# Performance work log

Hardware: AMD Instinct MI355X
Metric: run time of the kernel (lower is better)

The kernel has to match this reference:

```python
import jax, jax.numpy as jnp
import numpy as np

B, S, D = 8, 8192, 64
N_HASHES = 8
BUCKET_SIZE = 64
N_BUCKETS = S // BUCKET_SIZE  # 128
SELF_ATTN_VALUE = -5e4  # torch reformer TOKEN_SELF_ATTN_VALUE


def setup_inputs() -> dict:
    key = jax.random.key(0)
    k1, k2, k3 = jax.random.split(key, 3)
    qk = jax.random.normal(k1, (B, S, D), dtype=jnp.float32)
    v = jax.random.normal(k2, (B, S, D), dtype=jnp.float32)
    # LSH random rotations: (dim, n_hashes, n_buckets // 2), shared across batch/heads
    rotations = jax.random.normal(k3, (D, N_HASHES, N_BUCKETS // 2), dtype=jnp.float32)
    return {"qk": qk, "v": v, "rotations": rotations, "query_len": S}


def _look_one_back(x):
    # concatenate each chunk with the preceding chunk (wrapping) along the kv axis
    x_extra = jnp.concatenate([x[:, -1:], x[:, :-1]], axis=1)
    return jnp.concatenate([x, x_extra], axis=2)


def _lsh_bucketed_dots(qk, v, rotations):
    batch, seqlen, dim = qk.shape
    n_buckets = seqlen // BUCKET_SIZE
    # --- hash vectors: rotate, concat with negation, argmax -> bucket ids ---
    rotated = jnp.einsum('btf,fhi->bhti', qk, rotations)           # (B, H, S, nb/2)
    rotated = jnp.concatenate([rotated, -rotated], axis=-1)        # (B, H, S, nb)
    buckets = jnp.argmax(rotated, axis=-1)                         # (B, H, S) int
    offsets = (jnp.arange(N_HASHES) * n_buckets)[None, :, None]    # disjoint per round
    buckets = (buckets + offsets).reshape(batch, -1)               # (B, H*S)

    # --- stable bucket sort via composite key (all keys unique) ---
    ticker = jnp.arange(N_HASHES * seqlen)[None, :]                # (1, H*S)
    buckets_and_t = seqlen * buckets + (ticker % seqlen)
    sticker = jnp.argsort(buckets_and_t, axis=-1)                  # sort permutation
    undo_sort = jnp.argsort(sticker, axis=-1)                      # inverse permutation
    st = sticker % seqlen                                          # original token ids

    # --- gather tokens into bucket order ---
    sqk = jnp.take_along_axis(qk, st[..., None], axis=1)           # (B, H*S, D)
    sv = jnp.take_along_axis(v, st[..., None], axis=1)

    n_chunks = N_HASHES * n_buckets
    bq_t = st.reshape(batch, n_chunks, BUCKET_SIZE)                # (B, C, bs)
    bqk = sqk.reshape(batch, n_chunks, BUCKET_SIZE, dim)
    bv = sv.reshape(batch, n_chunks, BUCKET_SIZE, dim)

    bq = bqk
    bk = bqk / (jnp.linalg.norm(bqk, axis=-1, keepdims=True) + 1e-6)  # unit-length keys

    bk = _look_one_back(bk)       # (B, C, 2*bs, D)
    bv = _look_one_back(bv)
    bkv_t = _look_one_back(bq_t)  # (B, C, 2*bs)

    dots = jnp.einsum('buie,buje->buij', bq, bk) * (dim ** -0.5)   # (B, C, bs, 2*bs)
    self_mask = bq_t[:, :, :, None] == bkv_t[:, :, None, :]
    dots = jnp.where(self_mask, SELF_ATTN_VALUE, dots)
    return dots, undo_sort, bv


def reference(qk, v, rotations, query_len):
    batch, seqlen, dim = qk.shape
    dots, undo_sort, bv = _lsh_bucketed_dots(qk, v, rotations)
    dots_logsumexp = jax.nn.logsumexp(dots, axis=-1, keepdims=True)
    p = jnp.exp(dots - dots_logsumexp)                             # per-bucket softmax
    bo = jnp.einsum('buij,buje->buie', p, bv)                      # (B, C, bs, D)
    so = bo.reshape(batch, -1, dim)                                # (B, H*S, D)
    slogits = dots_logsumexp.reshape(batch, -1)                    # (B, H*S)
    # undo the bucket sort
    o = jnp.take_along_axis(so, undo_sort[..., None], axis=1)
    logits = jnp.take_along_axis(slogits, undo_sort, axis=1)
    o = o.reshape(batch, N_HASHES, seqlen, dim)[:, :, :query_len]
    logits = logits.reshape(batch, N_HASHES, seqlen, 1)[:, :, :query_len]
    # combine across hash rounds, weighted by per-round logsumexp
    probs = jnp.exp(logits - jax.nn.logsumexp(logits, axis=1, keepdims=True))
    out = jnp.sum(o * probs, axis=1)                               # (B, query_len, D)
    return out
```

## Files before the change

### kernel.cpp

```cpp
#include <hip/hip_runtime.h>
#include <math.h>

#define B_  8
#define S_  8192
#define D_  64
#define H_  8
#define NB_ 128
#define NC_ 1024
#define REP_CAP 65536
#define T2_ 2e-3f

typedef _Float16 f16x8 __attribute__((ext_vector_type(8)));
typedef _Float16 f16x2 __attribute__((ext_vector_type(2)));
typedef float    f32x4 __attribute__((ext_vector_type(4)));
typedef unsigned int uint_;

#define MFMA16(A, Bv, C) __builtin_amdgcn_mfma_f32_16x16x32_f16(A, Bv, C, 0, 0, 0)

__global__ __launch_bounds__(256) void prep_rot_kernel(
    const float* __restrict__ rot, _Float16* __restrict__ rotHi,
    _Float16* __restrict__ rotLo, int* __restrict__ cnt)
{
  __shared__ float rs[64 * 64];
  const int tid = threadIdx.x, h = blockIdx.x;
  if (h == 0 && tid == 0) *cnt = 0;
#pragma unroll
  for (int it = 0; it < 16; ++it) {
    const int f = it * 4 + (tid >> 6), i = tid & 63;
    rs[f * 64 + i] = rot[f * 512 + h * 64 + i];
  }
  __syncthreads();
  const int i = tid & 63, grp = tid >> 6;
  _Float16 hi[16], lo[16];
#pragma unroll
  for (int ff = 0; ff < 16; ++ff) {
    const float x = rs[(grp * 16 + ff) * 64 + i];
    hi[ff] = (_Float16)x;
    lo[ff] = (_Float16)(x - (float)hi[ff]);
  }
  f16x8* dH = (f16x8*)(rotHi + h * 4096 + i * 64 + grp * 16);
  f16x8* dL = (f16x8*)(rotLo + h * 4096 + i * 64 + grp * 16);
  dH[0] = ((f16x8*)hi)[0]; dH[1] = ((f16x8*)hi)[1];
  dL[0] = ((f16x8*)lo)[0]; dL[1] = ((f16x8*)lo)[1];
}

__global__ __launch_bounds__(256) void prep_tok_kernel(
    const float* __restrict__ qk, const float* __restrict__ v,
    _Float16* __restrict__ q16, _Float16* __restrict__ kn16,
    _Float16* __restrict__ v16)
{
  const int gt = blockIdx.x * 64 + (threadIdx.x >> 2);
  const int qu = threadIdx.x & 3;
  const size_t off = (size_t)gt * 64 + qu * 16;
  float x[16];
#pragma unroll
  for (int k = 0; k < 4; ++k) ((float4*)x)[k] = ((const float4*)(qk + off))[k];
  float ss = 0.f;
#pragma unroll
  for (int k = 0; k < 16; ++k) ss = fmaf(x[k], x[k], ss);
  ss += __shfl_xor(ss, 1); ss += __shfl_xor(ss, 2);
  const float inv = 0.125f / (sqrtf(ss) + 1e-6f);
  f16x8 qh[2], kn[2];
#pragma unroll
  for (int j = 0; j < 16; ++j) {
    qh[j >> 3][j & 7] = (_Float16)x[j];
    kn[j >> 3][j & 7] = (_Float16)(x[j] * inv);
  }
  ((f16x8*)(q16  + off))[0] = qh[0]; ((f16x8*)(q16  + off))[1] = qh[1];
  ((f16x8*)(kn16 + off))[0] = kn[0]; ((f16x8*)(kn16 + off))[1] = kn[1];
  float y[16];
#pragma unroll
  for (int k = 0; k < 4; ++k) ((float4*)y)[k] = ((const float4*)(v + off))[k];
  f16x8 vv[2];
#pragma unroll
  for (int j = 0; j < 16; ++j) vv[j >> 3][j & 7] = (_Float16)y[j];
  ((f16x8*)(v16 + off))[0] = vv[0]; ((f16x8*)(v16 + off))[1] = vv[1];
}

__global__ __launch_bounds__(256) void hash_kernel(
    const float* __restrict__ qk,
    const _Float16* __restrict__ rotHi, const _Float16* __restrict__ rotLo,
    int* __restrict__ bucket, int* __restrict__ cnt, int2* __restrict__ list)
{
  __shared__ _Float16 rH[64 * 72];
  __shared__ _Float16 rL[64 * 72];
  const int tid  = threadIdx.x;
  const int tile = blockIdx.x & 127;
  const int b    = blockIdx.x >> 7;
  const int lane = tid & 63, w = tid >> 6;
  const int m16  = lane & 15, qd = lane >> 4;

  const int t = tile * 64 + w * 16 + m16;
  f16x8 BH0, BH1, BL0, BL1;
  {
    const float* src = qk + ((size_t)b * S_ + t) * 64 + 8 * qd;
    float x[16];
    ((float4*)x)[0] = ((const float4*)src)[0];
    ((float4*)x)[1] = ((const float4*)(src + 4))[0];
    ((float4*)x)[2] = ((const float4*)(src + 32))[0];
    ((float4*)x)[3] = ((const float4*)(src + 36))[0];
#pragma unroll
    for (int j = 0; j < 8; ++j) {
      const _Float16 h0 = (_Float16)x[j];
      BH0[j] = h0; BL0[j] = (_Float16)(x[j] - (float)h0);
      const _Float16 h1 = (_Float16)x[j + 8];
      BH1[j] = h1; BL1[j] = (_Float16)(x[j + 8] - (float)h1);
    }
  }
  const int srow = tid >> 2, scol = (tid & 3) * 16;
  const uint_ qd16 = (uint_)(qd << 4);

#pragma unroll 1
  for (int h = 0; h < 8; ++h) {
    __syncthreads();
    {
      const _Float16* sH = rotHi + h * 4096 + srow * 64 + scol;
      const _Float16* sL = rotLo + h * 4096 + srow * 64 + scol;
      *(f16x8*)(rH + srow * 72 + scol)     = ((const f16x8*)sH)[0];
      *(f16x8*)(rH + srow * 72 + scol + 8) = ((const f16x8*)sH)[1];
      *(f16x8*)(rL + srow * 72 + scol)     = ((const f16x8*)sL)[0];
      *(f16x8*)(rL + srow * 72 + scol + 8) = ((const f16x8*)sL)[1];
    }
    __syncthreads();

    f32x4 acc[4];
#pragma unroll
    for (int mt = 0; mt < 4; ++mt) acc[mt] = (f32x4){0.f, 0.f, 0.f, 0.f};
#pragma unroll
    for (int mt = 0; mt < 4; ++mt) {
      const _Float16* aH = rH + (16 * mt + m16) * 72 + 8 * qd;
      const _Float16* aL = rL + (16 * mt + m16) * 72 + 8 * qd;
      const f16x8 AH0 = *(const f16x8*)aH;
      const f16x8 AH1 = *(const f16x8*)(aH + 32);
      const f16x8 AL0 = *(const f16x8*)aL;
      const f16x8 AL1 = *(const f16x8*)(aL + 32);
      acc[mt] = MFMA16(AH0, BH0, acc[mt]);
      acc[mt] = MFMA16(AH1, BH1, acc[mt]);
      acc[mt] = MFMA16(AH0, BL0, acc[mt]);
      acc[mt] = MFMA16(AH1, BL1, acc[mt]);
      acc[mt] = MFMA16(AL0, BH0, acc[mt]);
      acc[mt] = MFMA16(AL1, BH1, acc[mt]);
    }

    float v1M = -1e30f, v2M = -1e30f, v1m = 1e30f, v2m = 1e30f;
#pragma unroll
    for (int mt = 0; mt < 4; ++mt)
#pragma unroll
      for (int rg = 0; rg < 4; ++rg) {
        uint_ u = __float_as_uint(acc[mt][rg]);
        u = (u & 0xFFFFFFC0u) | qd16 | (uint_)((mt << 2) | rg);
        const float xk = __uint_as_float(u);
        v2M = __builtin_amdgcn_fmed3f(v1M, v2M, xk);
        v1M = fmaxf(v1M, xk);
        v2m = __builtin_amdgcn_fmed3f(v1m, v2m, xk);
        v1m = fminf(v1m, xk);
      }
#pragma unroll
    for (int off = 16; off <= 32; off <<= 1) {
      const float o1M = __shfl_xor(v1M, off), o2M = __shfl_xor(v2M, off);
      v2M = __builtin_amdgcn_fmed3f(v1M, o1M, fmaxf(v2M, o2M));
      v1M = fmaxf(v1M, o1M);
      const float o1m = __shfl_xor(v1m, off), o2m = __shfl_xor(v2m, off);
      v2m = __builtin_amdgcn_fmed3f(v1m, o1m, fminf(v2m, o2m));
      v1m = fminf(v1m, o1m);
    }
    if (qd == 0) {
      const uint_ cM = __float_as_uint(v1M) & 63u;
      const uint_ cm = __float_as_uint(v1m) & 63u;
      const int ixM = 16 * (int)((cM >> 2) & 3u) + 4 * (int)(cM >> 4) + (int)(cM & 3u);
      const int ixm = 16 * (int)((cm >> 2) & 3u) + 4 * (int)(cm >> 4) + (int)(cm & 3u);
      const int bkt = (v1M >= -v1m) ? ixM : 64 + ixm;
      bucket[((size_t)(b * 8 + h)) * S_ + t] = bkt;
      const bool flag = ((v1M - v2M) < T2_) | ((v2m - v1m) < T2_) |
                        (fabsf(v1M + v1m) < T2_);
      if (flag) {
        const int s = atomicAdd(cnt, 1);
        if (s < REP_CAP) list[s] = make_int2(b * 8 + h, t);
      }
    }
  }
}

__global__ __launch_bounds__(256) void repair_kernel(
    const float* __restrict__ qk, const float* __restrict__ rot,
    const int* __restrict__ cnt, const int2* __restrict__ list,
    int* __restrict__ bucket)
{
  const int n = min(*cnt, REP_CAP);
  const int lane = threadIdx.x & 63;
  const int wid  = (blockIdx.x * 256 + threadIdx.x) >> 6;
  const int nw   = gridDim.x * 4;
  for (int idx = wid; idx < n; idx += nw) {
    const int bh = list[idx].x, t = list[idx].y;
    const int b = bh >> 3, hh = bh & 7;
    const float* qrow = qk + ((size_t)b * S_ + t) * D_;
    const float* rcol = rot + hh * 64 + lane;
    double acc = 0.0;
#pragma unroll 8
    for (int f = 0; f < 64; ++f)
      acc = fma((double)qrow[f], (double)rcol[(size_t)f * 512], acc);
    double vM = acc; int iM = lane;
    double vm = acc; int im = lane;
#pragma unroll
    for (int off = 32; off >= 1; off >>= 1) {
      const double voM = __shfl_xor(vM, off); const int ioM = __shfl_xor(iM, off);
      if (voM > vM || (voM == vM && ioM < iM)) { vM = voM; iM = ioM; }
      const double vom = __shfl_xor(vm, off); const int iom = __shfl_xor(im, off);
      if (vom < vm || (vom == vm && iom < im)) { vm = vom; im = iom; }
    }
    if (lane == 0) {
      const int bkt = (vM >= -vm) ? iM : 64 + im;
      bucket[(size_t)bh * S_ + t] = bkt;
    }
  }
}

__global__ __launch_bounds__(1024) void sort_kernel(
    const int* __restrict__ bucket, int* __restrict__ st)
{
  __shared__ uint_ hist[64 * 128];
  __shared__ unsigned short lb[S_];
  __shared__ int off[128];
  const int tid = threadIdx.x;
  const int bh  = blockIdx.x;
  const size_t base = (size_t)bh * S_;

#pragma unroll
  for (int k = 0; k < 8; ++k) hist[tid + k * 1024] = 0;
  __syncthreads();

#pragma unroll
  for (int k = 0; k < 8; ++k) {
    const int t = k * 1024 + tid;
    const int bk = bucket[base + t];
    lb[t] = (unsigned short)bk;
    const int g = t >> 6;
    atomicAdd(&hist[(g & 63) * 128 + bk], 1u << (16 * (g >> 6)));
  }
  __syncthreads();

  if (tid < 128) {
    uint_ s = 0;
#pragma unroll
    for (int g = 0; g < 64; ++g) {
      const uint_ wv = hist[g * 128 + tid];
      s += (wv & 0xFFFFu) + (wv >> 16);
    }
    off[tid] = (int)s;
  }
  __syncthreads();
  if (tid == 0) {
    int run = 0;
    for (int k = 0; k < 128; ++k) { const int c = off[k]; off[k] = run; run += c; }
  }
  __syncthreads();
  if (tid < 128) {
    uint_ run = (uint_)off[tid];
#pragma unroll
    for (int g = 0; g < 64; ++g) {
      const uint_ wv = hist[g * 128 + tid];
      hist[g * 128 + tid] = (wv & 0xFFFF0000u) | run;
      run += (wv & 0xFFFFu);
    }
#pragma unroll
    for (int g = 0; g < 64; ++g) {
      const uint_ wv = hist[g * 128 + tid];
      hist[g * 128 + tid] = (wv & 0xFFFFu) | (run << 16);
      run += (wv >> 16);
    }
  }
  __syncthreads();

  const int lane = tid & 63, wv_ = tid >> 6;
  const int b = bh >> 3, h = bh & 7;
  const size_t stb = (size_t)b * (H_ * S_) + (size_t)h * S_;
  const unsigned long long ltmask = (1ull << lane) - 1ull;
#pragma unroll
  for (int k = 0; k < 8; ++k) {
    const int g = wv_ * 8 + k;
    const int t = g * 64 + lane;
    const int bk = (int)lb[t];
    unsigned long long same = ~0ull;
#pragma unroll
    for (int bit = 0; bit < 7; ++bit) {
      const unsigned long long m = __ballot((bk >> bit) & 1);
      same &= ((bk >> bit) & 1) ? m : ~m;
    }
    const int rloc = __popcll(same & ltmask);
    const uint_ wd = hist[(g & 63) * 128 + bk];
    const int gbase = (int)((wd >> (16 * (g >> 6))) & 0xFFFFu);
    st[stb + gbase + rloc] = t;
  }
}

__global__ __launch_bounds__(256, 4) void attn_kernel(
    const _Float16* __restrict__ q16, const _Float16* __restrict__ kn16,
    const _Float16* __restrict__ v16, const int* __restrict__ st,
    _Float16* __restrict__ so, float* __restrict__ slog)
{
  __shared__ _Float16 sQ[64 * 72];
  __shared__ _Float16 sK[64 * 72];
  __shared__ _Float16 sP[64 * 136];
  __shared__ int sIds[128];

  const int tid = threadIdx.x;
  const int c   = blockIdx.x & (NC_ - 1);
  const int b   = blockIdx.x >> 10;
  const int cm1 = (c + NC_ - 1) & (NC_ - 1);
  const size_t bst = (size_t)b * (H_ * S_);
  const size_t row0 = bst + (size_t)c * 64;
  const size_t row1 = bst + (size_t)cm1 * 64;

  const int lane = tid & 63;
  const int w    = tid >> 6;
  const int m16  = lane & 15;
  const int qd   = lane >> 4;

  if (tid < 128) sIds[tid] = (tid < 64) ? st[row0 + tid] : st[row1 + tid - 64];

  const int r = tid >> 2, qu = tid & 3;
  {
    const int tok = st[row0 + r];
    const size_t go = ((size_t)b * S_ + tok) * 64 + qu * 16;
    const f16x8* sq = (const f16x8*)(q16 + go);
    *(f16x8*)(sQ + r * 72 + qu * 16)     = sq[0];
    *(f16x8*)(sQ + r * 72 + qu * 16 + 8) = sq[1];
    const f16x8* sk = (const f16x8*)(kn16 + go);
    *(f16x8*)(sK + r * 72 + qu * 16)     = sk[0];
    *(f16x8*)(sK + r * 72 + qu * 16 + 8) = sk[1];
  }
  __syncthreads();

  f32x4 acc[8];
#pragma unroll
  for (int jt = 0; jt < 8; ++jt) acc[jt] = (f32x4){0.f, 0.f, 0.f, 0.f};

  const _Float16* qrow = sQ + (16 * w + m16) * 72;
  const f16x8 a0 = *(const f16x8*)(qrow + 8 * qd);
  const f16x8 a1 = *(const f16x8*)(qrow + 32 + 8 * qd);

#pragma unroll
  for (int jt = 0; jt < 4; ++jt) {
    const _Float16* krow = sK + (16 * jt + m16) * 72;
    const f16x8 b0 = *(const f16x8*)(krow + 8 * qd);
    const f16x8 b1 = *(const f16x8*)(krow + 32 + 8 * qd);
    acc[jt] = MFMA16(a0, b0, acc[jt]);
    acc[jt] = MFMA16(a1, b1, acc[jt]);
  }
  __syncthreads();

  {
    const int tok = st[row1 + r];
    const f16x8* sk = (const f16x8*)(kn16 + ((size_t)b * S_ + tok) * 64 + qu * 16);
    *(f16x8*)(sK + r * 72 + qu * 16)     = sk[0];
    *(f16x8*)(sK + r * 72 + qu * 16 + 8) = sk[1];
  }
  __syncthreads();

#pragma unroll
  for (int jt = 4; jt < 8; ++jt) {
    const _Float16* krow = sK + (16 * (jt - 4) + m16) * 72;
    const f16x8 b0 = *(const f16x8*)(krow + 8 * qd);
    const f16x8 b1 = *(const f16x8*)(krow + 32 + 8 * qd);
    acc[jt] = MFMA16(a0, b0, acc[jt]);
    acc[jt] = MFMA16(a1, b1, acc[jt]);
  }

  const int jp = tid >> 2;
  const int tok0 = sIds[2 * jp], tok1 = sIds[2 * jp + 1];
  f16x8 va[2], vb[2];
  {
    const f16x8* s0 = (const f16x8*)(v16 + ((size_t)b * S_ + tok0) * 64 + qu * 16);
    const f16x8* s1 = (const f16x8*)(v16 + ((size_t)b * S_ + tok1) * 64 + qu * 16);
    va[0] = s0[0]; va[1] = s0[1];
    vb[0] = s1[0]; vb[1] = s1[1];
  }

  int rid[4];
#pragma unroll
  for (int rg = 0; rg < 4; ++rg) rid[rg] = sIds[16 * w + 4 * qd + rg];
  float rmax[4] = {-1e30f, -1e30f, -1e30f, -1e30f};
#pragma unroll
  for (int jt = 0; jt < 8; ++jt) {
    const int cid = sIds[16 * jt + m16];
#pragma unroll
    for (int rg = 0; rg < 4; ++rg) {
      float x = acc[jt][rg];
      if (rid[rg] == cid) x = -5e4f;
      acc[jt][rg] = x;
      rmax[rg] = fmaxf(rmax[rg], x);
    }
  }
#pragma unroll
  for (int rg = 0; rg < 4; ++rg) {
    rmax[rg] = fmaxf(rmax[rg], __shfl_xor(rmax[rg], 1));
    rmax[rg] = fmaxf(rmax[rg], __shfl_xor(rmax[rg], 2));
    rmax[rg] = fmaxf(rmax[rg], __shfl_xor(rmax[rg], 4));
    rmax[rg] = fmaxf(rmax[rg], __shfl_xor(rmax[rg], 8));
  }
  float rsum[4] = {0.f, 0.f, 0.f, 0.f};
#pragma unroll
  for (int jt = 0; jt < 8; ++jt)
#pragma unroll
    for (int rg = 0; rg < 4; ++rg) {
      const float e = __expf(acc[jt][rg] - rmax[rg]);
      acc[jt][rg] = e;
      rsum[rg] += e;
    }
#pragma unroll
  for (int rg = 0; rg < 4; ++rg) {
    rsum[rg] += __shfl_xor(rsum[rg], 1);
    rsum[rg] += __shfl_xor(rsum[rg], 2);
    rsum[rg] += __shfl_xor(rsum[rg], 4);
    rsum[rg] += __shfl_xor(rsum[rg], 8);
  }
  float rinv[4];
#pragma unroll
  for (int rg = 0; rg < 4; ++rg) rinv[rg] = 1.f / rsum[rg];

  const int hh = c >> 7;
  const size_t hb = ((size_t)(b * 8 + hh)) * S_;
  if (m16 == 0) {
#pragma unroll
    for (int rg = 0; rg < 4; ++rg)
      slog[hb + rid[rg]] = rmax[rg] + __logf(rsum[rg]);
  }

#pragma unroll
  for (int jt = 0; jt < 8; ++jt)
#pragma unroll
    for (int rg = 0; rg < 4; ++rg)
      sP[(16 * w + 4 * qd + rg) * 136 + 16 * jt + m16] = (_Float16)acc[jt][rg];

  __syncthreads();

  {
    const int j = 2 * jp;
    _Float16* dst = (j < 64) ? (sK + j) : (sQ + (j - 64));
#pragma unroll
    for (int jj = 0; jj < 16; ++jj) {
      const int d = qu * 16 + jj;
      f16x2 pk; pk[0] = va[jj >> 3][jj & 7]; pk[1] = vb[jj >> 3][jj & 7];
      *(f16x2*)(dst + d * 72) = pk;
    }
  }
  __syncthreads();

  f32x4 oacc[4];
#pragma unroll
  for (int dt = 0; dt < 4; ++dt) oacc[dt] = (f32x4){0.f, 0.f, 0.f, 0.f};
  const _Float16* prow = sP + (16 * w + m16) * 136;
#pragma unroll
  for (int s = 0; s < 4; ++s) {
    const f16x8 ap = *(const f16x8*)(prow + 32 * s + 8 * qd);
    const _Float16* vbase = (s < 2) ? sK : sQ;
    const int col0 = 32 * (s & 1) + 8 * qd;
#pragma unroll
    for (int dt = 0; dt < 4; ++dt) {
      const f16x8 bv = *(const f16x8*)(vbase + (16 * dt + m16) * 72 + col0);
      oacc[dt] = MFMA16(ap, bv, oacc[dt]);
    }
  }

#pragma unroll
  for (int dt = 0; dt < 4; ++dt)
#pragma unroll
    for (int rg = 0; rg < 4; ++rg)
      so[(hb + rid[rg]) * 64 + 16 * dt + m16] = (_Float16)(oacc[dt][rg] * rinv[rg]);
}

__global__ __launch_bounds__(256) void combine_kernel(
    const _Float16* __restrict__ so, const float* __restrict__ slog,
    float* __restrict__ out)
{
  const int gt = blockIdx.x * 4 + (threadIdx.x >> 6);
  const int d  = threadIdx.x & 63;
  const int b  = gt >> 13;
  const int t  = gt & (S_ - 1);

  float l[8];
#pragma unroll
  for (int h = 0; h < 8; ++h)
    l[h] = slog[((size_t)(b * 8 + h)) * S_ + t];
  float m = l[0];
#pragma unroll
  for (int h = 1; h < 8; ++h) m = fmaxf(m, l[h]);
  float wv[8], W = 0.f;
#pragma unroll
  for (int h = 0; h < 8; ++h) { wv[h] = expf(l[h] - m); W += wv[h]; }
  const float iW = 1.f / W;
  float acc = 0.f;
#pragma unroll
  for (int h = 0; h < 8; ++h)
    acc = fmaf(wv[h], (float)so[(((size_t)(b * 8 + h)) * S_ + t) * 64 + d], acc);
  out[(size_t)gt * 64 + d] = acc * iW;
}

extern "C" void kernel_launch(void* const* d_in, const int* in_sizes, int n_in,
                              void* d_out, int out_size, void* d_ws, size_t ws_size,
                              hipStream_t stream)
{
  const float* qk  = (const float*)d_in[0];
  const float* v   = (const float*)d_in[1];
  const float* rot = (const float*)d_in[2];
  float* out = (float*)d_out;

  char* ws = (char*)d_ws;
  const size_t MB = 1ull << 20, KB = 1024;
  int*      bucket = (int*)      (ws + 0 * MB);
  int*      st     = (int*)      (ws + 2 * MB);
  float*    slog   = (float*)    (ws + 4 * MB);
  _Float16* q16    = (_Float16*) (ws + 8 * MB);
  _Float16* kn16   = (_Float16*) (ws + 16 * MB);
  _Float16* v16    = (_Float16*) (ws + 24 * MB);
  _Float16* rotHi  = (_Float16*) (ws + 32 * MB);
  _Float16* rotLo  = (_Float16*) (ws + 32 * MB + 64 * KB);
  int*      cnt    = (int*)      (ws + 32 * MB + 128 * KB);
  int2*     list   = (int2*)     (ws + 32 * MB + 192 * KB);
  _Float16* so     = (_Float16*) (ws + 33 * MB);
  if (ws_size < 98 * MB) return;

  hipLaunchKernelGGL(prep_rot_kernel, dim3(8),           dim3(256),  0, stream, rot, rotHi, rotLo, cnt);
  hipLaunchKernelGGL(prep_tok_kernel, dim3(1024),        dim3(256),  0, stream, qk, v, q16, kn16, v16);
  hipLaunchKernelGGL(hash_kernel,     dim3(8 * 128),     dim3(256),  0, stream, qk, rotHi, rotLo, bucket, cnt, list);
  hipLaunchKernelGGL(repair_kernel,   dim3(128),         dim3(256),  0, stream, qk, rot, cnt, list, bucket);
  hipLaunchKernelGGL(sort_kernel,     dim3(64),          dim3(1024), 0, stream, bucket, st);
  hipLaunchKernelGGL(attn_kernel,     dim3(B_ * NC_),    dim3(256),  0, stream, q16, kn16, v16, st, so, slog);
  hipLaunchKernelGGL(combine_kernel,  dim3(B_ * S_ / 4), dim3(256),  0, stream, so, slog, out);
}
```

Baseline: 207.1 us.

## Restructure attention kernel to keep P in registers and shrink shared memory

The attention kernel now computes the transposed score tile (K as the A operand, Q from registers), so each lane holds a full query row's scores. This lets the softmax reduction use two cross-quad shuffles instead of four per row and lets P be fed straight into the PV MFMA from registers, with no sP staging. Shared memory drops to one reused buffer with a swizzled transposed-V layout, and launch bounds rise to 8 blocks per CU for higher occupancy. In exchange the register permutation and swizzle indexing are harder to follow, and register pressure under the tighter bound may cause spills.

```diff
diff --git a/kernel.cpp b/kernel.cpp
--- a/kernel.cpp
+++ b/kernel.cpp
@@ -293,15 +293,13 @@
   }
 }
 
-__global__ __launch_bounds__(256, 4) void attn_kernel(
+__global__ __launch_bounds__(256, 8) void attn_kernel(
     const _Float16* __restrict__ q16, const _Float16* __restrict__ kn16,
     const _Float16* __restrict__ v16, const int* __restrict__ st,
     _Float16* __restrict__ so, float* __restrict__ slog)
 {
-  __shared__ _Float16 sQ[64 * 72];
-  __shared__ _Float16 sK[64 * 72];
-  __shared__ _Float16 sP[64 * 136];
-  __shared__ int sIds[128];
+  __shared__ _Float16 smem[64 * 136];
+  __shared__ __align__(16) int sIds[128];
 
   const int tid = threadIdx.x;
   const int c   = blockIdx.x & (NC_ - 1);
@@ -318,16 +316,20 @@
 
   if (tid < 128) sIds[tid] = (tid < 64) ? st[row0 + tid] : st[row1 + tid - 64];
 
+  const int rid = st[row0 + 16 * w + m16];
+  f16x8 q0, q1;
+  {
+    const _Float16* qp = q16 + ((size_t)b * S_ + rid) * 64 + 8 * qd;
+    q0 = *(const f16x8*)qp;
+    q1 = *(const f16x8*)(qp + 32);
+  }
+
   const int r = tid >> 2, qu = tid & 3;
   {
     const int tok = st[row0 + r];
-    const size_t go = ((size_t)b * S_ + tok) * 64 + qu * 16;
-    const f16x8* sq = (const f16x8*)(q16 + go);
-    *(f16x8*)(sQ + r * 72 + qu * 16)     = sq[0];
-    *(f16x8*)(sQ + r * 72 + qu * 16 + 8) = sq[1];
-    const f16x8* sk = (const f16x8*)(kn16 + go);
-    *(f16x8*)(sK + r * 72 + qu * 16)     = sk[0];
-    *(f16x8*)(sK + r * 72 + qu * 16 + 8) = sk[1];
+    const f16x8* sk = (const f16x8*)(kn16 + ((size_t)b * S_ + tok) * 64 + qu * 16);
+    *(f16x8*)(smem + r * 72 + qu * 16)     = sk[0];
+    *(f16x8*)(smem + r * 72 + qu * 16 + 8) = sk[1];
   }
   __syncthreads();
 
@@ -335,39 +337,73 @@
 #pragma unroll
   for (int jt = 0; jt < 8; ++jt) acc[jt] = (f32x4){0.f, 0.f, 0.f, 0.f};
 
-  const _Float16* qrow = sQ + (16 * w + m16) * 72;
-  const f16x8 a0 = *(const f16x8*)(qrow + 8 * qd);
-  const f16x8 a1 = *(const f16x8*)(qrow + 32 + 8 * qd);
-
 #pragma unroll
   for (int jt = 0; jt < 4; ++jt) {
-    const _Float16* krow = sK + (16 * jt + m16) * 72;
-    const f16x8 b0 = *(const f16x8*)(krow + 8 * qd);
-    const f16x8 b1 = *(const f16x8*)(krow + 32 + 8 * qd);
-    acc[jt] = MFMA16(a0, b0, acc[jt]);
-    acc[jt] = MFMA16(a1, b1, acc[jt]);
+    const _Float16* krow = smem + (16 * jt + m16) * 72;
+    const f16x8 kb0 = *(const f16x8*)(krow + 8 * qd);
+    const f16x8 kb1 = *(const f16x8*)(krow + 32 + 8 * qd);
+    acc[jt] = MFMA16(kb0, q0, acc[jt]);
+    acc[jt] = MFMA16(kb1, q1, acc[jt]);
   }
   __syncthreads();
 
   {
-    const int tok = st[row1 + r];
+    const int tok = sIds[64 + r];
     const f16x8* sk = (const f16x8*)(kn16 + ((size_t)b * S_ + tok) * 64 + qu * 16);
-    *(f16x8*)(sK + r * 72 + qu * 16)     = sk[0];
-    *(f16x8*)(sK + r * 72 + qu * 16 + 8) = sk[1];
+    *(f16x8*)(smem + r * 72 + qu * 16)     = sk[0];
+    *(f16x8*)(smem + r * 72 + qu * 16 + 8) = sk[1];
   }
   __syncthreads();
 
 #pragma unroll
   for (int jt = 4; jt < 8; ++jt) {
-    const _Float16* krow = sK + (16 * (jt - 4) + m16) * 72;
-    const f16x8 b0 = *(const f16x8*)(krow + 8 * qd);
-    const f16x8 b1 = *(const f16x8*)(krow + 32 + 8 * qd);
-    acc[jt] = MFMA16(a0, b0, acc[jt]);
-    acc[jt] = MFMA16(a1, b1, acc[jt]);
-  }
-
-  const int jp = tid >> 2;
-  const int tok0 = sIds[2 * jp], tok1 = sIds[2 * jp + 1];
+    const _Float16* krow = smem + (16 * (jt - 4) + m16) * 72;
+    const f16x8 kb0 = *(const f16x8*)(krow + 8 * qd);
+    const f16x8 kb1 = *(const f16x8*)(krow + 32 + 8 * qd);
+    acc[jt] = MFMA16(kb0, q0, acc[jt]);
+    acc[jt] = MFMA16(kb1, q1, acc[jt]);
+  }
+
+  float m = -1e30f;
+#pragma unroll
+  for (int jt = 0; jt < 8; ++jt) {
+    const int4 cid = *(const int4*)(sIds + 16 * jt + 4 * qd);
+    float x;
+    x = acc[jt][0]; if (cid.x == rid) x = -5e4f; acc[jt][0] = x; m = fmaxf(m, x);
+    x = acc[jt][1]; if (cid.y == rid) x = -5e4f; acc[jt][1] = x; m = fmaxf(m, x);
+    x = acc[jt][2]; if (cid.z == rid) x = -5e4f; acc[jt][2] = x; m = fmaxf(m, x);
+    x = acc[jt][3]; if (cid.w == rid) x = -5e4f; acc[jt][3] = x; m = fmaxf(m, x);
+  }
+  m = fmaxf(m, __shfl_xor(m, 16));
+  m = fmaxf(m, __shfl_xor(m, 32));
+  float sum = 0.f;
+#pragma unroll
+  for (int jt = 0; jt < 8; ++jt)
+#pragma unroll
+    for (int rg = 0; rg < 4; ++rg) {
+      const float e = __expf(acc[jt][rg] - m);
+      acc[jt][rg] = e;
+      sum += e;
+    }
+  sum += __shfl_xor(sum, 16);
+  sum += __shfl_xor(sum, 32);
+  const float rinv = 1.f / sum;
+
+  const int hh = c >> 7;
+  const size_t hb = ((size_t)(b * 8 + hh)) * S_;
+  if (qd == 0) slog[hb + rid] = m + __logf(sum);
+
+  f16x8 pa[4];
+#pragma unroll
+  for (int s = 0; s < 4; ++s)
+#pragma unroll
+    for (int j = 0; j < 8; ++j)
+      pa[s][j] = (_Float16)acc[2 * s + (j >> 2)][j & 3];
+
+  const int jp = r;
+  const int c0 = 2 * jp;
+  const int k0 = 32 * (c0 >> 5) + 16 * ((c0 >> 2) & 1) + 4 * ((c0 >> 3) & 3) + (c0 & 3);
+  const int tok0 = sIds[k0], tok1 = sIds[k0 + 1];
   f16x8 va[2], vb[2];
   {
     const f16x8* s0 = (const f16x8*)(v16 + ((size_t)b * S_ + tok0) * 64 + qu * 16);
@@ -375,98 +411,44 @@
     va[0] = s0[0]; va[1] = s0[1];
     vb[0] = s1[0]; vb[1] = s1[1];
   }
-
-  int rid[4];
-#pragma unroll
-  for (int rg = 0; rg < 4; ++rg) rid[rg] = sIds[16 * w + 4 * qd + rg];
-  float rmax[4] = {-1e30f, -1e30f, -1e30f, -1e30f};
-#pragma unroll
-  for (int jt = 0; jt < 8; ++jt) {
-    const int cid = sIds[16 * jt + m16];
-#pragma unroll
-    for (int rg = 0; rg < 4; ++rg) {
-      float x = acc[jt][rg];
-      if (rid[rg] == cid) x = -5e4f;
-      acc[jt][rg] = x;
-      rmax[rg] = fmaxf(rmax[rg], x);
-    }
-  }
-#pragma unroll
-  for (int rg = 0; rg < 4; ++rg) {
-    rmax[rg] = fmaxf(rmax[rg], __shfl_xor(rmax[rg], 1));
-    rmax[rg] = fmaxf(rmax[rg], __shfl_xor(rmax[rg], 2));
-    rmax[rg] = fmaxf(rmax[rg], __shfl_xor(rmax[rg], 4));
-    rmax[rg] = fmaxf(rmax[rg], __shfl_xor(rmax[rg], 8));
-  }
-  float rsum[4] = {0.f, 0.f, 0.f, 0.f};
-#pragma unroll
-  for (int jt = 0; jt < 8; ++jt)
-#pragma unroll
-    for (int rg = 0; rg < 4; ++rg) {
-      const float e = __expf(acc[jt][rg] - rmax[rg]);
-      acc[jt][rg] = e;
-      rsum[rg] += e;
-    }
-#pragma unroll
-  for (int rg = 0; rg < 4; ++rg) {
-    rsum[rg] += __shfl_xor(rsum[rg], 1);
-    rsum[rg] += __shfl_xor(rsum[rg], 2);
-    rsum[rg] += __shfl_xor(rsum[rg], 4);
-    rsum[rg] += __shfl_xor(rsum[rg], 8);
-  }
-  float rinv[4];
-#pragma unroll
-  for (int rg = 0; rg < 4; ++rg) rinv[rg] = 1.f / rsum[rg];
-
-  const int hh = c >> 7;
-  const size_t hb = ((size_t)(b * 8 + hh)) * S_;
-  if (m16 == 0) {
+  __syncthreads();
+
+  {
+    const int swz = (qu << 3) ^ ((qu & 1) << 5);
+    _Float16* dst = smem + (c0 ^ swz);
+#pragma unroll
+    for (int jj = 0; jj < 16; ++jj) {
+      const int d = 16 * qu + jj;
+      f16x2 pk; pk[0] = va[jj >> 3][jj & 7]; pk[1] = vb[jj >> 3][jj & 7];
+      *(f16x2*)(dst + d * 136) = pk;
+    }
+  }
+  __syncthreads();
+
+  f32x4 oacc[4];
+#pragma unroll
+  for (int dt = 0; dt < 4; ++dt) oacc[dt] = (f32x4){0.f, 0.f, 0.f, 0.f};
+#pragma unroll
+  for (int s = 0; s < 4; ++s) {
+#pragma unroll
+    for (int dt = 0; dt < 4; ++dt) {
+      const _Float16* vp = smem + (16 * dt + m16) * 136
+                         + 32 * (s ^ (dt & 1)) + 8 * (qd ^ dt);
+      const f16x8 bv = *(const f16x8*)vp;
+      oacc[dt] = MFMA16(pa[s], bv, oacc[dt]);
+    }
+  }
+
+  const int4 rid4 = *(const int4*)(sIds + 16 * w + 4 * qd);
+  const int ridv[4] = {rid4.x, rid4.y, rid4.z, rid4.w};
+  float rin[4];
+#pragma unroll
+  for (int rg = 0; rg < 4; ++rg) rin[rg] = __shfl(rinv, 4 * qd + rg);
+#pragma unroll
+  for (int dt = 0; dt < 4; ++dt)
 #pragma unroll
     for (int rg = 0; rg < 4; ++rg)
-      slog[hb + rid[rg]] = rmax[rg] + __logf(rsum[rg]);
-  }
-
-#pragma unroll
-  for (int jt = 0; jt < 8; ++jt)
-#pragma unroll
-    for (int rg = 0; rg < 4; ++rg)
-      sP[(16 * w + 4 * qd + rg) * 136 + 16 * jt + m16] = (_Float16)acc[jt][rg];
-
-  __syncthreads();
-
-  {
-    const int j = 2 * jp;
-    _Float16* dst = (j < 64) ? (sK + j) : (sQ + (j - 64));
-#pragma unroll
-    for (int jj = 0; jj < 16; ++jj) {
-      const int d = qu * 16 + jj;
-      f16x2 pk; pk[0] = va[jj >> 3][jj & 7]; pk[1] = vb[jj >> 3][jj & 7];
-      *(f16x2*)(dst + d * 72) = pk;
-    }
-  }
-  __syncthreads();
-
-  f32x4 oacc[4];
-#pragma unroll
-  for (int dt = 0; dt < 4; ++dt) oacc[dt] = (f32x4){0.f, 0.f, 0.f, 0.f};
-  const _Float16* prow = sP + (16 * w + m16) * 136;
-#pragma unroll
-  for (int s = 0; s < 4; ++s) {
-    const f16x8 ap = *(const f16x8*)(prow + 32 * s + 8 * qd);
-    const _Float16* vbase = (s < 2) ? sK : sQ;
-    const int col0 = 32 * (s & 1) + 8 * qd;
-#pragma unroll
-    for (int dt = 0; dt < 4; ++dt) {
-      const f16x8 bv = *(const f16x8*)(vbase + (16 * dt + m16) * 72 + col0);
-      oacc[dt] = MFMA16(ap, bv, oacc[dt]);
-    }
-  }
-
-#pragma unroll
-  for (int dt = 0; dt < 4; ++dt)
-#pragma unroll
-    for (int rg = 0; rg < 4; ++rg)
-      so[(hb + rid[rg]) * 64 + 16 * dt + m16] = (_Float16)(oacc[dt][rg] * rinv[rg]);
+      so[(hb + ridv[rg]) * 64 + 16 * dt + m16] = (_Float16)(oacc[dt][rg] * rin[rg]);
 }
 
 __global__ __launch_bounds__(256) void combine_kernel(
```

Result: faster. 195.0 us (-5.9%).
